# Optimization experiments

Hardware: AMD Instinct MI355X
Metric: run time of the kernel (lower is better)

The kernel has to match this reference:

```python
import jax, jax.numpy as jnp
import numpy as np

HID = 64  # hidden_dim


def _w(k, shape, fan):
    # torch default: U(-1/sqrt(hidden), 1/sqrt(hidden))
    bound = 1.0 / np.sqrt(fan)
    return jax.random.uniform(k, shape, jnp.float32, -bound, bound)


def setup_inputs() -> dict:
    key = jax.random.key(0)
    ks = jax.random.split(key, 16)
    B, L, S, D = 32, 168, 512, 1
    H = HID
    return {
        "x_seq": jax.random.normal(ks[0], (B, L, S, D), jnp.float32),
        # encoder LSTM layer 0 (input_size=D)
        "W_ih0": _w(ks[1], (4 * H, D), H), "W_hh0": _w(ks[2], (4 * H, H), H),
        "b_ih0": _w(ks[3], (4 * H,), H), "b_hh0": _w(ks[4], (4 * H,), H),
        # encoder LSTM layer 1 (input_size=H)
        "W_ih1": _w(ks[5], (4 * H, H), H), "W_hh1": _w(ks[6], (4 * H, H), H),
        "b_ih1": _w(ks[7], (4 * H,), H), "b_hh1": _w(ks[8], (4 * H,), H),
        # decoder LSTMCell (input_size=D)
        "Wc_ih": _w(ks[9], (4 * H, D), H), "Wc_hh": _w(ks[10], (4 * H, H), H),
        "bc_ih": _w(ks[11], (4 * H,), H), "bc_hh": _w(ks[12], (4 * H,), H),
        # output projection hidden -> input_dim
        "W_out": _w(ks[13], (D, H), H), "b_out": _w(ks[14], (D,), H),
        "horizon": 24,
    }


def _cell(x, h, c, Wih, Whh, bih, bhh):
    # torch gate order: i, f, g, o
    g = x @ Wih.T + bih + h @ Whh.T + bhh  # (N, 4H)
    i, f, gg, o = jnp.split(g, 4, axis=-1)
    c = jax.nn.sigmoid(f) * c + jax.nn.sigmoid(i) * jnp.tanh(gg)
    h = jax.nn.sigmoid(o) * jnp.tanh(c)
    return h, c


def _lstm_layer(x, Wih, Whh, bih, bhh):
    # x: (N, L, D_in) -> outputs (N, L, H), final h, c
    N = x.shape[0]
    Hd = Whh.shape[1]
    init = (jnp.zeros((N, Hd), x.dtype), jnp.zeros((N, Hd), x.dtype))

    def step(carry, xt):
        h, c = carry
        h, c = _cell(xt, h, c, Wih, Whh, bih, bhh)
        return (h, c), h

    (h, c), ys = jax.lax.scan(step, init, jnp.swapaxes(x, 0, 1))
    return jnp.swapaxes(ys, 0, 1), h, c


def reference(x_seq, W_ih0, W_hh0, b_ih0, b_hh0, W_ih1, W_hh1, b_ih1, b_hh1,
              Wc_ih, Wc_hh, bc_ih, bc_hh, W_out, b_out, horizon):
    B, L, S, D = x_seq.shape
    # (B, L, S, D) -> (B*S, L, D)
    x = jnp.transpose(x_seq, (0, 2, 1, 3)).reshape(B * S, L, D)
    # 2-layer encoder LSTM; dropout is identity in eval mode
    y1, _, _ = _lstm_layer(x, W_ih0, W_hh0, b_ih0, b_hh0)
    _, h, c = _lstm_layer(y1, W_ih1, W_hh1, b_ih1, b_hh1)
    x_cur = x[:, -1, :]

    def dec(carry, _):
        h, c, xc = carry
        h, c = _cell(xc, h, c, Wc_ih, Wc_hh, bc_ih, bc_hh)
        y = h @ W_out.T + b_out  # (N, D)
        return (h, c, y), y

    _, ys = jax.lax.scan(dec, (h, c, x_cur), None, length=horizon)  # (Hor, N, D)
    y = jnp.transpose(ys, (1, 0, 2)).reshape(B, S, horizon, D)
    return jnp.transpose(y, (0, 2, 1, 3))  # (B, Hor, S, D)
```

## Files before the change

### kernel.cpp

```cpp
#include <hip/hip_runtime.h>

typedef __attribute__((ext_vector_type(8))) short short8;
typedef __attribute__((ext_vector_type(4))) float f32x4;

#define MFMA16(a, b, c) __builtin_amdgcn_mfma_f32_16x16x32_bf16((a), (b), (c), 0, 0, 0)

constexpr int Bv  = 32;
constexpr int Lv  = 168;
constexpr int Sv  = 512;
constexpr int HZv = 24;
constexpr int Mv  = 64;
constexpr int HSTR = 88;
constexpr int HBUF = Mv * HSTR;

__device__ __forceinline__ float b2f(short s) {
    unsigned u = ((unsigned)(unsigned short)s) << 16;
    return __builtin_bit_cast(float, u);
}
__device__ __forceinline__ short f2b(float f) {
    unsigned u = __builtin_bit_cast(unsigned, f);
    unsigned r = (u + 0x7FFFu + ((u >> 16) & 1u)) >> 16;
    return (short)(unsigned short)r;
}
__device__ __forceinline__ float sigm(float x) {
    float e = __builtin_amdgcn_exp2f(-1.44269504088896f * x);
    return __builtin_amdgcn_rcpf(1.0f + e);
}
__device__ __forceinline__ float tanh_(float x) {
    float e = __builtin_amdgcn_exp2f(2.88539008177793f * x);
    return 1.0f - 2.0f * __builtin_amdgcn_rcpf(e + 1.0f);
}
__device__ __forceinline__ void hi8(const float* __restrict__ p, short8& hi) {
#pragma unroll
    for (int j = 0; j < 8; ++j) hi[j] = f2b(p[j]);
}

__global__ __launch_bounds__(512)
void sitewise_lstm(const float* __restrict__ x_seq,
                   const float* __restrict__ Wih0, const float* __restrict__ Whh0,
                   const float* __restrict__ bih0, const float* __restrict__ bhh0,
                   const float* __restrict__ Wih1, const float* __restrict__ Whh1,
                   const float* __restrict__ bih1, const float* __restrict__ bhh1,
                   const float* __restrict__ Wcih, const float* __restrict__ Wchh,
                   const float* __restrict__ bcih, const float* __restrict__ bchh,
                   const float* __restrict__ Wout, const float* __restrict__ bout,
                   float* __restrict__ out)
{
    __shared__ __align__(16) short Hhi[4 * HBUF];
    __shared__ float woutF[64];
    __shared__ float ybufF[Mv];

    const int tid  = threadIdx.x;
    const int wv   = tid >> 6;
    const int lane = tid & 63;
    const int q    = lane >> 4;
    const int col  = lane & 15;
    const int mh   = wv >> 2;
    const int U    = wv & 3;
    const int bid  = blockIdx.x;
    const int b    = bid >> 3;
    const int s0   = (bid & 7) << 6;
    const int uu   = U * 16 + col;
    const int me   = mh * 32 + q * 4;

    for (int i = tid; i < 4 * HBUF / 2; i += 512) ((int*)Hhi)[i] = 0;
    if (tid < 64) woutF[tid] = Wout[tid];

    const float* xbF = x_seq + b * Lv * Sv + s0;

    const int roA = ((mh * 2 + 0) * 16 + col) * HSTR + q * 8;
    const int wiA = (me) * HSTR + uu;

    short8 Whi[3][4][2];
    float bias0[4], bias1[4], biasc[4], wih0gE[4], wcihgE[4];
#pragma unroll
    for (int g = 0; g < 4; ++g) {
        const int j = g * 64 + U * 16 + col;
        bias0[g] = bih0[j] + bhh0[j];
        bias1[g] = bih1[j] + bhh1[j];
        biasc[g] = bcih[j] + bchh[j];
#pragma unroll
        for (int kc = 0; kc < 2; ++kc) {
            const int off = j * 64 + kc * 32 + q * 8;
            hi8(Whh0 + off, Whi[0][g][kc]);
            hi8(Wih1 + off, Whi[1][g][kc]);
            hi8(Whh1 + off, Whi[2][g][kc]);
        }
        wih0gE[g] = Wih0[g * 64 + uu];
        wcihgE[g] = Wcih[g * 64 + uu];
    }

    float c0[8], c1[8];
#pragma unroll
    for (int i = 0; i < 8; ++i) { c0[i] = 0.f; c1[i] = 0.f; }

    __syncthreads();

#define ENC_STEP(T, B0P, B0N, B1P, B1N) do {                                          \
        f32x4 xv[2];                                                                  \
        xv[0] = *(const f32x4*)(xbF + (T) * Sv + me);                                 \
        xv[1] = *(const f32x4*)(xbF + (T) * Sv + me + 16);                            \
        short8 ah[2][2];                                                              \
        _Pragma("unroll")                                                             \
        for (int kc = 0; kc < 2; ++kc)                                                \
            _Pragma("unroll")                                                         \
            for (int mt = 0; mt < 2; ++mt)                                            \
                ah[kc][mt] = *(const short8*)(Hhi + (B0P) + roA + kc * 32 + mt * 16 * HSTR); \
        f32x4 pre0[4][2];                                                             \
        _Pragma("unroll")                                                             \
        for (int g = 0; g < 4; ++g)                                                   \
            _Pragma("unroll")                                                         \
            for (int mt = 0; mt < 2; ++mt)                                            \
                pre0[g][mt] = (f32x4){bias0[g], bias0[g], bias0[g], bias0[g]};        \
        _Pragma("unroll")                                                             \
        for (int g = 0; g < 4; ++g)                                                   \
            _Pragma("unroll")                                                         \
            for (int mt = 0; mt < 2; ++mt) pre0[g][mt] = MFMA16(ah[0][mt], Whi[0][g][0], pre0[g][mt]); \
        _Pragma("unroll")                                                             \
        for (int g = 0; g < 4; ++g)                                                   \
            _Pragma("unroll")                                                         \
            for (int mt = 0; mt < 2; ++mt) pre0[g][mt] = MFMA16(ah[1][mt], Whi[0][g][1], pre0[g][mt]); \
        _Pragma("unroll")                                                             \
        for (int mt = 0; mt < 2; ++mt)                                                \
            _Pragma("unroll")                                                         \
            for (int r = 0; r < 4; ++r) {                                             \
                const float xw = xv[mt][r];                                           \
                const float ig = sigm (pre0[0][mt][r] + xw * wih0gE[0]);              \
                const float fg = sigm (pre0[1][mt][r] + xw * wih0gE[1]);              \
                const float gt = tanh_(pre0[2][mt][r] + xw * wih0gE[2]);              \
                const float og = sigm (pre0[3][mt][r] + xw * wih0gE[3]);              \
                const float c  = fg * c0[mt * 4 + r] + ig * gt;                       \
                c0[mt * 4 + r] = c;                                                   \
                Hhi[(B0N) + wiA + (mt * 16 + r) * HSTR] = f2b(og * tanh_(c));         \
            }                                                                         \
        __syncthreads();                       \
        short8 bh[2][2], dh[2][2];                                                    \
        _Pragma("unroll")                                                             \
        for (int kc = 0; kc < 2; ++kc)                                                \
            _Pragma("unroll")                                                         \
            for (int mt = 0; mt < 2; ++mt) {                                          \
                bh[kc][mt] = *(const short8*)(Hhi + (B0N) + roA + kc * 32 + mt * 16 * HSTR); \
                dh[kc][mt] = *(const short8*)(Hhi + (B1P) + roA + kc * 32 + mt * 16 * HSTR); \
            }                                                                         \
        f32x4 pre1[4][2];                                                             \
        _Pragma("unroll")                                                             \
        for (int g = 0; g < 4; ++g)                                                   \
            _Pragma("unroll")                                                         \
            for (int mt = 0; mt < 2; ++mt)                                            \
                pre1[g][mt] = (f32x4){bias1[g], bias1[g], bias1[g], bias1[g]};        \
        _Pragma("unroll")                                                             \
        for (int g = 0; g < 4; ++g)                                                   \
            _Pragma("unroll")                                                         \
            for (int mt = 0; mt < 2; ++mt) pre1[g][mt] = MFMA16(bh[0][mt], Whi[1][g][0], pre1[g][mt]); \
        _Pragma("unroll")                                                             \
        for (int g = 0; g < 4; ++g)                                                   \
            _Pragma("unroll")                                                         \
            for (int mt = 0; mt < 2; ++mt) pre1[g][mt] = MFMA16(bh[1][mt], Whi[1][g][1], pre1[g][mt]); \
        _Pragma("unroll")                                                             \
        for (int g = 0; g < 4; ++g)                                                   \
            _Pragma("unroll")                                                         \
            for (int mt = 0; mt < 2; ++mt) pre1[g][mt] = MFMA16(dh[0][mt], Whi[2][g][0], pre1[g][mt]); \
        _Pragma("unroll")                                                             \
        for (int g = 0; g < 4; ++g)                                                   \
            _Pragma("unroll")                                                         \
            for (int mt = 0; mt < 2; ++mt) pre1[g][mt] = MFMA16(dh[1][mt], Whi[2][g][1], pre1[g][mt]); \
        _Pragma("unroll")                                                             \
        for (int mt = 0; mt < 2; ++mt)                                                \
            _Pragma("unroll")                                                         \
            for (int r = 0; r < 4; ++r) {                                             \
                const float ig = sigm (pre1[0][mt][r]);                               \
                const float fg = sigm (pre1[1][mt][r]);                               \
                const float gt = tanh_(pre1[2][mt][r]);                               \
                const float og = sigm (pre1[3][mt][r]);                               \
                const float c  = fg * c1[mt * 4 + r] + ig * gt;                       \
                c1[mt * 4 + r] = c;                                                   \
                Hhi[(B1N) + wiA + (mt * 16 + r) * HSTR] = f2b(og * tanh_(c));         \
            }                                                                         \
             \
             \
    } while (0)

    for (int t = 0; t < Lv; t += 2) {
        ENC_STEP(t,     0 * HBUF, 1 * HBUF, 2 * HBUF, 3 * HBUF);
        ENC_STEP(t + 1, 1 * HBUF, 0 * HBUF, 3 * HBUF, 2 * HBUF);
    }
#undef ENC_STEP

#pragma unroll
    for (int g = 0; g < 4; ++g)
#pragma unroll
        for (int kc = 0; kc < 2; ++kc)
            hi8(Wchh + (g * 64 + U * 16 + col) * 64 + kc * 32 + q * 8, Whi[0][g][kc]);
    if (tid < Mv) ybufF[tid] = xbF[(Lv - 1) * Sv + tid];
    __syncthreads();

    const float boutF = bout[0];
    float* outp = out + b * HZv * Sv + s0;

#define DEC_STEP(T, B1P, B1N) do {                                                    \
        short8 ah[2][2];                                                              \
        _Pragma("unroll")                                                             \
        for (int kc = 0; kc < 2; ++kc)                                                \
            _Pragma("unroll")                                                         \
            for (int mt = 0; mt < 2; ++mt)                                            \
                ah[kc][mt] = *(const short8*)(Hhi + (B1P) + roA + kc * 32 + mt * 16 * HSTR); \
        float yv[2][4];                                                               \
        _Pragma("unroll")                                                             \
        for (int mt = 0; mt < 2; ++mt)                                                \
            _Pragma("unroll")                                                         \
            for (int r = 0; r < 4; ++r)                                               \
                yv[mt][r] = ybufF[me + mt * 16 + r];                                  \
        f32x4 prc[4][2];                                                              \
        _Pragma("unroll")                                                             \
        for (int g = 0; g < 4; ++g)                                                   \
            _Pragma("unroll")                                                         \
            for (int mt = 0; mt < 2; ++mt)                                            \
                prc[g][mt] = (f32x4){biasc[g], biasc[g], biasc[g], biasc[g]};         \
        _Pragma("unroll")                                                             \
        for (int g = 0; g < 4; ++g)                                                   \
            _Pragma("unroll")                                                         \
            for (int mt = 0; mt < 2; ++mt) prc[g][mt] = MFMA16(ah[0][mt], Whi[0][g][0], prc[g][mt]); \
        _Pragma("unroll")                                                             \
        for (int g = 0; g < 4; ++g)                                                   \
            _Pragma("unroll")                                                         \
            for (int mt = 0; mt < 2; ++mt) prc[g][mt] = MFMA16(ah[1][mt], Whi[0][g][1], prc[g][mt]); \
        _Pragma("unroll")                                                             \
        for (int mt = 0; mt < 2; ++mt)                                                \
            _Pragma("unroll")                                                         \
            for (int r = 0; r < 4; ++r) {                                             \
                const float xw = yv[mt][r];                                           \
                const float ig = sigm (prc[0][mt][r] + xw * wcihgE[0]);               \
                const float fg = sigm (prc[1][mt][r] + xw * wcihgE[1]);               \
                const float gt = tanh_(prc[2][mt][r] + xw * wcihgE[2]);               \
                const float og = sigm (prc[3][mt][r] + xw * wcihgE[3]);               \
                const float c  = fg * c1[mt * 4 + r] + ig * gt;                       \
                c1[mt * 4 + r] = c;                                                   \
                Hhi[(B1N) + wiA + (mt * 16 + r) * HSTR] = f2b(og * tanh_(c));         \
            }                                                                         \
        __syncthreads();                                                              \
        if (tid < Mv) {                                                               \
            const int m = tid;                                                        \
            float s = boutF;                                                          \
            _Pragma("unroll")                                                         \
            for (int k = 0; k < 64; ++k)                                              \
                s += b2f(Hhi[(B1N) + m * HSTR + k]) * woutF[k];                       \
            outp[(T) * Sv + m] = s;                                                   \
            ybufF[m] = s;                                                             \
        }                                                                             \
        __syncthreads();                                                              \
    } while (0)

    for (int t = 0; t < HZv; t += 2) {
        DEC_STEP(t,     2 * HBUF, 3 * HBUF);
        DEC_STEP(t + 1, 3 * HBUF, 2 * HBUF);
    }
#undef DEC_STEP
}

extern "C" void kernel_launch(void* const* d_in, const int* in_sizes, int n_in,
                              void* d_out, int out_size, void* d_ws, size_t ws_size,
                              hipStream_t stream)
{
    const float* x_seq = (const float*)d_in[0];
    const float* Wih0  = (const float*)d_in[1];
    const float* Whh0  = (const float*)d_in[2];
    const float* bih0  = (const float*)d_in[3];
    const float* bhh0  = (const float*)d_in[4];
    const float* Wih1  = (const float*)d_in[5];
    const float* Whh1  = (const float*)d_in[6];
    const float* bih1  = (const float*)d_in[7];
    const float* bhh1  = (const float*)d_in[8];
    const float* Wcih  = (const float*)d_in[9];
    const float* Wchh  = (const float*)d_in[10];
    const float* bcih  = (const float*)d_in[11];
    const float* bchh  = (const float*)d_in[12];
    const float* Wout  = (const float*)d_in[13];
    const float* bout  = (const float*)d_in[14];
    float* out = (float*)d_out;

    hipLaunchKernelGGL(sitewise_lstm, dim3(Bv * (Sv / Mv)), dim3(512), 0, stream,
                       x_seq, Wih0, Whh0, bih0, bhh0, Wih1, Whh1, bih1, bhh1,
                       Wcih, Wchh, bcih, bchh, Wout, bout, out);
}
```

Measured before the change: 538.3 us.

## Halve per-block site tile to 32 with 256-thread blocks and split output projection

Each block now handles 32 sites with 4 waves (one per hidden-unit slice) instead of 64 sites with 8 waves, doubling the grid to 512 blocks. Shared memory is padded with a large dummy array, apparently to control how many blocks fit per CU, and launch bounds request 2 waves-per-EU. The decoder's output projection is split across 4 threads per site with shuffle reductions instead of one thread looping over 64 elements. The intent is better load balance across CUs and a shorter serial tail in the decoder, at the cost of more blocks and fewer rows per MFMA tile.

```diff
diff --git a/kernel.cpp b/kernel.cpp
--- a/kernel.cpp
+++ b/kernel.cpp
@@ -9,9 +9,10 @@
 constexpr int Lv  = 168;
 constexpr int Sv  = 512;
 constexpr int HZv = 24;
-constexpr int Mv  = 64;
+constexpr int Mv  = 32;
 constexpr int HSTR = 88;
 constexpr int HBUF = Mv * HSTR;
+constexpr int PADv = 16000;
 
 __device__ __forceinline__ float b2f(short s) {
     unsigned u = ((unsigned)(unsigned short)s) << 16;
@@ -35,7 +36,7 @@
     for (int j = 0; j < 8; ++j) hi[j] = f2b(p[j]);
 }
 
-__global__ __launch_bounds__(512)
+__global__ __launch_bounds__(256, 2)
 void sitewise_lstm(const float* __restrict__ x_seq,
                    const float* __restrict__ Wih0, const float* __restrict__ Whh0,
                    const float* __restrict__ bih0, const float* __restrict__ bhh0,
@@ -46,7 +47,7 @@
                    const float* __restrict__ Wout, const float* __restrict__ bout,
                    float* __restrict__ out)
 {
-    __shared__ __align__(16) short Hhi[4 * HBUF];
+    __shared__ __align__(16) short Hhi[4 * HBUF + PADv];
     __shared__ float woutF[64];
     __shared__ float ybufF[Mv];
 
@@ -55,27 +56,26 @@
     const int lane = tid & 63;
     const int q    = lane >> 4;
     const int col  = lane & 15;
-    const int mh   = wv >> 2;
-    const int U    = wv & 3;
+    const int U    = wv;
     const int bid  = blockIdx.x;
-    const int b    = bid >> 3;
-    const int s0   = (bid & 7) << 6;
+    const int b    = bid >> 4;
+    const int s0   = (bid & 15) << 5;
     const int uu   = U * 16 + col;
-    const int me   = mh * 32 + q * 4;
-
-    for (int i = tid; i < 4 * HBUF / 2; i += 512) ((int*)Hhi)[i] = 0;
+    const int me   = q * 4;
+
+    for (int i = tid; i < 4 * HBUF / 2; i += 256) ((int*)Hhi)[i] = 0;
     if (tid < 64) woutF[tid] = Wout[tid];
 
     const float* xbF = x_seq + b * Lv * Sv + s0;
 
-    const int roA = ((mh * 2 + 0) * 16 + col) * HSTR + q * 8;
-    const int wiA = (me) * HSTR + uu;
+    const int roA = col * HSTR + q * 8;
+    const int wiA = me * HSTR + uu;
 
     short8 Whi[3][4][2];
     float bias0[4], bias1[4], biasc[4], wih0gE[4], wcihgE[4];
 #pragma unroll
     for (int g = 0; g < 4; ++g) {
-        const int j = g * 64 + U * 16 + col;
+        const int j = g * 64 + uu;
         bias0[g] = bih0[j] + bhh0[j];
         bias1[g] = bih1[j] + bhh1[j];
         biasc[g] = bcih[j] + bchh[j];
@@ -86,8 +86,8 @@
             hi8(Wih1 + off, Whi[1][g][kc]);
             hi8(Whh1 + off, Whi[2][g][kc]);
         }
-        wih0gE[g] = Wih0[g * 64 + uu];
-        wcihgE[g] = Wcih[g * 64 + uu];
+        wih0gE[g] = Wih0[j];
+        wcihgE[g] = Wcih[j];
     }
 
     float c0[8], c1[8];
@@ -190,7 +190,7 @@
     for (int g = 0; g < 4; ++g)
 #pragma unroll
         for (int kc = 0; kc < 2; ++kc)
-            hi8(Wchh + (g * 64 + U * 16 + col) * 64 + kc * 32 + q * 8, Whi[0][g][kc]);
+            hi8(Wchh + (g * 64 + uu) * 64 + kc * 32 + q * 8, Whi[0][g][kc]);
     if (tid < Mv) ybufF[tid] = xbF[(Lv - 1) * Sv + tid];
     __syncthreads();
 
@@ -237,17 +237,23 @@
                 c1[mt * 4 + r] = c;                                                   \
                 Hhi[(B1N) + wiA + (mt * 16 + r) * HSTR] = f2b(og * tanh_(c));         \
             }                                                                         \
-        __syncthreads();                                                              \
-        if (tid < Mv) {                                                               \
-            const int m = tid;                                                        \
-            float s = boutF;                                                          \
-            _Pragma("unroll")                                                         \
-            for (int k = 0; k < 64; ++k)                                              \
-                s += b2f(Hhi[(B1N) + m * HSTR + k]) * woutF[k];                       \
-            outp[(T) * Sv + m] = s;                                                   \
-            ybufF[m] = s;                                                             \
+        __syncthreads();                         \
+        if (tid < 128) {        \
+            const int m  = tid >> 2;                                                  \
+            const int pp = tid & 3;                                                   \
+            float s = 0.f;                                                            \
+            _Pragma("unroll")                                                         \
+            for (int k = 0; k < 16; ++k)                                              \
+                s += b2f(Hhi[(B1N) + m * HSTR + pp * 16 + k]) * woutF[pp * 16 + k];   \
+            s += __shfl_xor(s, 1, 64);                                                \
+            s += __shfl_xor(s, 2, 64);                                                \
+            if (pp == 0) {                                                            \
+                const float y = s + boutF;                                            \
+                outp[(T) * Sv + m] = y;                                               \
+                ybufF[m] = y;                                                         \
+            }                                                                         \
         }                                                                             \
-        __syncthreads();                                                              \
+        __syncthreads();                             \
     } while (0)
 
     for (int t = 0; t < HZv; t += 2) {
@@ -278,7 +284,7 @@
     const float* bout  = (const float*)d_in[14];
     float* out = (float*)d_out;
 
-    hipLaunchKernelGGL(sitewise_lstm, dim3(Bv * (Sv / Mv)), dim3(512), 0, stream,
+    hipLaunchKernelGGL(sitewise_lstm, dim3(Bv * (Sv / Mv)), dim3(256), 0, stream,
                        x_seq, Wih0, Whh0, bih0, bhh0, Wih1, Whh1, bih1, bhh1,
                        Wcih, Wchh, bcih, bchh, Wout, bout, out);
 }
```

Measured after the change: 529.4 us. No clear change (-1.7%).
